# Performance work log

Measured on AMD Instinct MI355X. Metric: run time of the kernel, lower is better.

## Reference

```python
import jax, jax.numpy as jnp
import numpy as np

B, C, H, W = 16, 256, 56, 56
HEADS, DHEAD = 8, 32
INNER = HEADS * DHEAD  # == C
BLOCK, HALO = 7, 3
WIN = BLOCK + 2 * HALO      # 13
REL = WIN                   # rel_size = block + 2*halo
HIDDEN = 4 * C
EPS = 1e-6
LS_INIT = 1e-6


def layernorm2d(x, w, b):
    # channels-first LayerNorm over C, x: (B,C,H,W)
    u = jnp.mean(x, axis=1, keepdims=True)
    s = jnp.mean((x - u) ** 2, axis=1, keepdims=True)
    xn = (x - u) * jax.lax.rsqrt(s + EPS)
    return w[None, :, None, None] * xn + b[None, :, None, None]


def rel_to_abs(x):
    # x: (b, l, 2r-1) -> (b, l, r)
    b, l, m = x.shape
    r = (m + 1) // 2
    x = jnp.pad(x, ((0, 0), (0, 0), (0, 1))).reshape(b, l * (m + 1))
    x = jnp.pad(x, ((0, 0), (0, m - l))).reshape(b, l + 1, m)
    return x[:, :l, -r:]


def relative_logits_1d(q, rel_k):
    # q: (b, h, w, d); rel_k: (2r-1, d) -> (b, h, r, w, r)
    b, h, w, _ = q.shape
    r = (rel_k.shape[0] + 1) // 2
    logits = jnp.einsum('bxyd,rd->bxyr', q, rel_k)
    logits = rel_to_abs(logits.reshape(b * h, w, -1)).reshape(b, h, w, r)
    return jnp.broadcast_to(logits[:, :, None], (b, h, r, w, r))


def rel_pos_bias(q, rel_h, rel_w):
    b = q.shape[0]
    r = (rel_w.shape[0] + 1) // 2
    q2 = q.reshape(b, BLOCK, BLOCK, DHEAD)
    lw = relative_logits_1d(q2, rel_w)                        # (b, x, i, y, j)
    lw = lw.transpose(0, 1, 3, 2, 4).reshape(b, BLOCK * BLOCK, r * r)
    lh = relative_logits_1d(q2.transpose(0, 2, 1, 3), rel_h)  # (b, y, i, x, j)
    lh = lh.transpose(0, 3, 1, 4, 2).reshape(b, BLOCK * BLOCK, r * r)
    return lw + lh


def halo_attention(x, wq, wkv, wo, bo, rel_h, rel_w):
    Bq, _, Hh, Ww = x.shape
    nh, nw = Hh // BLOCK, Ww // BLOCK
    nb = nh * nw
    # queries: non-overlapping blocks -> (B*nb, BLOCK^2, C)
    q_inp = x.reshape(Bq, C, nh, BLOCK, nw, BLOCK).transpose(0, 2, 4, 3, 5, 1)
    q_inp = q_inp.reshape(Bq * nb, BLOCK * BLOCK, C)
    # keys/values: overlapping haloed windows (like F.unfold with padding=HALO)
    xp = jnp.pad(x, ((0, 0), (0, 0), (HALO, HALO), (HALO, HALO)))
    rows = (jnp.arange(nh) * BLOCK)[:, None] + jnp.arange(WIN)
    cols = (jnp.arange(nw) * BLOCK)[:, None] + jnp.arange(WIN)
    kv = xp[:, :, rows][:, :, :, :, cols]
    kv = kv.transpose(0, 2, 4, 3, 5, 1).reshape(Bq * nb, WIN * WIN, C)
    q = q_inp @ wq.T
    k, v = jnp.split(kv @ wkv.T, 2, axis=-1)

    def split_heads(t):
        b2, n2, _ = t.shape
        return t.reshape(b2, n2, HEADS, DHEAD).transpose(0, 2, 1, 3).reshape(b2 * HEADS, n2, DHEAD)

    q, k, v = map(split_heads, (q, k, v))
    q = q * (DHEAD ** -0.5)
    sim = jnp.einsum('bid,bjd->bij', q, k) + rel_pos_bias(q, rel_h, rel_w)
    # mask out-of-bounds (zero-padded) halo positions
    onep = jnp.pad(jnp.ones((Hh, Ww), sim.dtype), ((HALO, HALO), (HALO, HALO)))
    m = (onep[rows][:, :, cols].transpose(0, 2, 1, 3).reshape(nb, WIN * WIN)) > 0
    sim = sim.reshape(Bq, nb, HEADS, BLOCK * BLOCK, WIN * WIN)
    sim = jnp.where(m[None, :, None, None, :], sim, -jnp.finfo(sim.dtype).max)
    sim = sim.reshape(Bq * nb * HEADS, BLOCK * BLOCK, WIN * WIN)
    attn = jax.nn.softmax(sim, axis=-1)
    out = jnp.einsum('bij,bjd->bid', attn, v)
    out = out.reshape(Bq * nb, HEADS, BLOCK * BLOCK, DHEAD).transpose(0, 2, 1, 3)
    out = out.reshape(Bq * nb, BLOCK * BLOCK, INNER) @ wo.T + bo
    out = out.reshape(Bq, nh, nw, BLOCK, BLOCK, C).transpose(0, 5, 1, 3, 2, 4)
    return out.reshape(Bq, C, Hh, Ww)


def _forward(x, ln1_w, ln1_b, ln2_w, ln2_b, wq, wkv, wo, bo, rel_h, rel_w,
             gamma1, gamma2, fc1_w, fc1_b, fc2_w, fc2_b):
    y = halo_attention(layernorm2d(x, ln1_w, ln1_b), wq, wkv, wo, bo, rel_h, rel_w)
    x = x + gamma1 * y  # drop_path = 0 -> identity
    z = layernorm2d(x, ln2_w, ln2_b).transpose(0, 2, 3, 1)  # NHWC
    z = jax.nn.gelu(z @ fc1_w.T + fc1_b, approximate=False)
    z = z @ fc2_w.T + fc2_b
    z = gamma2 * z
    return x + z.transpose(0, 3, 1, 2)


def setup_inputs() -> dict:
    key = jax.random.key(0)
    ks = jax.random.split(key, 8)
    n = lambda k, sh: jax.random.normal(k, sh, jnp.float32) * 0.02
    scale = DHEAD ** -0.5
    return dict(
        x=jax.random.normal(ks[0], (B, C, H, W), jnp.float32),
        ln1_w=jnp.ones((C,), jnp.float32), ln1_b=jnp.zeros((C,), jnp.float32),
        ln2_w=jnp.ones((C,), jnp.float32), ln2_b=jnp.zeros((C,), jnp.float32),
        wq=n(ks[1], (INNER, C)),
        wkv=n(ks[2], (2 * INNER, C)),
        wo=n(ks[3], (C, INNER)), bo=jnp.zeros((C,), jnp.float32),
        rel_h=jax.random.normal(ks[4], (2 * REL - 1, DHEAD), jnp.float32) * scale,
        rel_w=jax.random.normal(ks[5], (2 * REL - 1, DHEAD), jnp.float32) * scale,
        gamma1=jnp.full((1, C, 1, 1), LS_INIT, jnp.float32),
        gamma2=jnp.full((1, 1, 1, C), LS_INIT, jnp.float32),
        fc1_w=n(ks[6], (HIDDEN, C)), fc1_b=jnp.zeros((HIDDEN,), jnp.float32),
        fc2_w=n(ks[7], (C, HIDDEN)), fc2_b=jnp.zeros((C,), jnp.float32),
    )


def reference(x, ln1_w, ln1_b, ln2_w, ln2_b, wq, wkv, wo, bo, rel_h, rel_w,
              gamma1, gamma2, fc1_w, fc1_b, fc2_w, fc2_b):
    return _forward(x, ln1_w, ln1_b, ln2_w, ln2_b, wq, wkv, wo, bo, rel_h, rel_w,
                    gamma1, gamma2, fc1_w, fc1_b, fc2_w, fc2_b)
```

## Files before the change

### kernel.cpp

```cpp
#include <hip/hip_runtime.h>
#include <cmath>

#define DI __device__ __forceinline__

typedef unsigned short ushort_t;
typedef unsigned char u8;
typedef __attribute__((ext_vector_type(8))) short short8;
typedef __attribute__((ext_vector_type(8))) unsigned short ushort8;
typedef __attribute__((ext_vector_type(4))) unsigned short ushort4_t;
typedef __attribute__((ext_vector_type(4))) float floatx4;
typedef unsigned int u32;
typedef __attribute__((ext_vector_type(4))) u32 uintx4;

DI float bf2f(ushort_t u) {
    unsigned v = ((unsigned)u) << 16;
    float f;
    __builtin_memcpy(&f, &v, 4);
    return f;
}
DI ushort_t f2bf(float f) {
    unsigned u;
    __builtin_memcpy(&u, &f, 4);
    unsigned r = (u + 0x7FFFu + ((u >> 16) & 1u)) >> 16;
    return (ushort_t)r;
}
DI ushort_t f2bf_tr(float f) {
    unsigned u;
    __builtin_memcpy(&u, &f, 4);
    return (ushort_t)(u >> 16);
}
DI u32 pack2bf(float lo, float hi) {
    u32 a, b;
    __builtin_memcpy(&a, &lo, 4);
    __builtin_memcpy(&b, &hi, 4);
    return (a >> 16) | (b & 0xFFFF0000u);
}
DI u8 f2e4m3(float f) {
    u32 u;
    __builtin_memcpy(&u, &f, 4);
    u32 s = (u >> 24) & 0x80u;
    u32 a = u & 0x7FFFFFFFu;
    if (a < 0x3C800000u) return (u8)s;
    if (a >= 0x43E00000u) return (u8)(s | 0x7E);
    a += 0x7FFFFu + ((a >> 20) & 1u);
    u32 e = (a >> 23) - 120u;
    u32 m = (a >> 20) & 7u;
    return (u8)(s | (e << 3) | m);
}
DI u8 f2fp8(float v) {
#if __has_builtin(__builtin_amdgcn_cvt_pk_fp8_f32)
    return (u8)(__builtin_amdgcn_cvt_pk_fp8_f32(v, v, 0, false) & 0xFF);
#else
    return f2e4m3(v);
#endif
}
DI u32 pack4fp8(float v0, float v1, float v2, float v3) {
#if __has_builtin(__builtin_amdgcn_cvt_pk_fp8_f32)
    int p = __builtin_amdgcn_cvt_pk_fp8_f32(v0, v1, 0, false);
    p = __builtin_amdgcn_cvt_pk_fp8_f32(v2, v3, p, true);
    return (u32)p;
#else
    return (u32)f2e4m3(v0) | ((u32)f2e4m3(v1) << 8) | ((u32)f2e4m3(v2) << 16) |
           ((u32)f2e4m3(v3) << 24);
#endif
}

DI void async_copy16(const void* gsrc, void* ldst) {
    auto gp = (const __attribute__((address_space(1))) u32*)gsrc;
    auto lp = (__attribute__((address_space(3))) u32*)ldst;
    __builtin_amdgcn_global_load_lds(gp, lp, 16, 0, 0);
}


__global__ void convert_all_kernel(const float* __restrict__ wq, const float* __restrict__ wkv,
                                   const float* __restrict__ wo, const float* __restrict__ fc1w,
                                   const float* __restrict__ fc2w, const float* __restrict__ relh,
                                   const float* __restrict__ relw,
                                   ushort_t* __restrict__ bqkv, ushort_t* __restrict__ woC,
                                   u8* __restrict__ fc1C8, u8* __restrict__ fc2C8,
                                   ushort_t* __restrict__ relC, ushort_t* __restrict__ boneB) {
    int i = blockIdx.x * 256 + threadIdx.x;
    if (i < 196608) { bqkv[i] = f2bf(i < 65536 ? wq[i] : wkv[i - 65536]); return; }
    i -= 196608;
    if (i < 65536) { woC[i] = f2bf(wo[i]); return; }
    i -= 65536;
    if (i < 262144) { fc1C8[i] = f2fp8(fc1w[i]); return; }
    i -= 262144;
    if (i < 262144) { fc2C8[i] = f2fp8(fc2w[i]); return; }
    i -= 262144;
    if (i < 800) { relC[i] = f2bf(relh[i]); return; }
    i -= 800;
    if (i < 800) { relC[800 + i] = f2bf(relw[i]); return; }
    i -= 800;
    if (i < 5632) {
        int j = i >> 5, k = i & 31;
        int kh = j / 13, kw = j - kh * 13;
        ushort_t v = 0;
        if (j < 169) {
            if (k == kh || k == 13 + kw) v = 0x3F80;
            if (k == 28 && kh < 3) v = 0x3F80;
            if (k == 29 && kh >= 10) v = 0x3F80;
            if (k == 30 && kw < 3) v = 0x3F80;
            if (k == 31 && kw >= 10) v = 0x3F80;
        } else {
            if (k == 27) v = 0x3F80;
        }
        boneB[i] = v;
    }
}

__global__ __launch_bounds__(256) void ln1_kernel(const float* __restrict__ x,
                                                  const float* __restrict__ w,
                                                  const float* __restrict__ bias,
                                                  ushort_t* __restrict__ t1) {
    __shared__ __align__(16) float lds[56 * 256];
    int b = blockIdx.x / 56, h = blockIdx.x % 56;
    int c = threadIdx.x;
    const float* row = x + (((size_t)(b * 256 + c) * 56 + h) * 56);
    floatx4 vals[14];
#pragma unroll
    for (int i = 0; i < 14; i++) vals[i] = *(const floatx4*)(row + i * 4);
#pragma unroll
    for (int i = 0; i < 14; i++)
#pragma unroll
        for (int e = 0; e < 4; e++) lds[(i * 4 + e) * 256 + c] = vals[i][e];
    __syncthreads();
    int wv = threadIdx.x >> 6, lane = threadIdx.x & 63;
    for (int p0 = 0; p0 < 14; p0++) {
        int p = wv * 14 + p0;
        float xv[4];
        float s = 0.f, q = 0.f;
#pragma unroll
        for (int j = 0; j < 4; j++) {
            xv[j] = lds[p * 256 + lane * 4 + j];
            s += xv[j];
            q += xv[j] * xv[j];
        }
#pragma unroll
        for (int off = 32; off; off >>= 1) {
            s += __shfl_xor(s, off);
            q += __shfl_xor(q, off);
        }
        float mean = s * (1.f / 256.f);
        float var = q * (1.f / 256.f) - mean * mean;
        float rstd = rsqrtf(var + 1e-6f);
        size_t token = ((size_t)b * 56 + h) * 56 + p;
        ushort4_t o4;
#pragma unroll
        for (int j = 0; j < 4; j++) {
            int cc = lane * 4 + j;
            o4[j] = f2bf_tr(w[cc] * ((xv[j] - mean) * rstd) + bias[cc]);
        }
        *(ushort4_t*)(t1 + token * 256 + lane * 4) = o4;
    }
}

template <int EPI, int F8>
__global__ __launch_bounds__(256) void gemm_kernel(const void* __restrict__ A,
                                                   const void* __restrict__ Bw,
                                                   void* __restrict__ Cout, int K, int N,
                                                   const float* __restrict__ biasf,
                                                   const float* __restrict__ resf,
                                                   const float* __restrict__ gammaf,
                                                   int tok0) {
    constexpr int ES = F8 ? 1 : 2;
    constexpr bool SWAP = (EPI == 6);
    __shared__ __align__(16) char As[2][128 * 32 * ES];
    __shared__ __align__(16) char Bs[2][128 * 32 * ES];
    int gy = gridDim.y;
    int lin = blockIdx.y * gridDim.x + blockIdx.x;
    int chunk = (gridDim.x * gy) >> 3;
    int wl = (lin & 7) * chunk + (lin >> 3);
    int mt = wl / gy;
    int m0 = mt * 128, n0 = (wl - mt * gy) * 128;
    int t = threadIdx.x;
    int wave = t >> 6, lane = t & 63;
    int wm = (wave & 1) * 64, wn = (wave >> 1) * 64;
    int lr = lane & 15, quad = lane >> 4;
    floatx4 acc[4][4] = {};

    const char* A8 = (const char*)A;
    const char* B8 = (const char*)Bw;
    const size_t rbA = (size_t)K * ES;

    int cpr = 2 * ES;
    int r0 = t / cpr, o0 = (t % cpr) * 16;
    int r1 = (t + 256) / cpr, o1 = ((t + 256) % cpr) * 16;
    const char* Ar0 = A8 + (size_t)(m0 + r0) * rbA + o0;
    const char* Br0 = B8 + (size_t)(n0 + r0) * rbA + o0;
    const char* Ar1 = A8 + (size_t)(m0 + r1) * rbA + o1;
    const char* Br1 = B8 + (size_t)(n0 + r1) * rbA + o1;

    async_copy16(Ar0, &As[0][t * 16]);
    async_copy16(Br0, &Bs[0][t * 16]);
    if constexpr (!F8) {
        async_copy16(Ar1, &As[0][(t + 256) * 16]);
        async_copy16(Br1, &Bs[0][(t + 256) * 16]);
    }
    __syncthreads();

    int cur = 0;
    for (int k0 = 0; k0 < K; k0 += 32) {
        if (k0 + 32 < K) {
            size_t nb = (size_t)32 * ES;
            async_copy16(Ar0 + (k0 / 32 + 1) * nb, &As[cur ^ 1][t * 16]);
            async_copy16(Br0 + (k0 / 32 + 1) * nb, &Bs[cur ^ 1][t * 16]);
            if constexpr (!F8) {
                async_copy16(Ar1 + (k0 / 32 + 1) * nb, &As[cur ^ 1][(t + 256) * 16]);
                async_copy16(Br1 + (k0 / 32 + 1) * nb, &Bs[cur ^ 1][(t + 256) * 16]);
            }
        }
        if constexpr (F8) {
            long af[4], bf[4];
#pragma unroll
            for (int i = 0; i < 4; i++)
                __builtin_memcpy(&af[i], &As[cur][(wm + i * 16 + lr) * 32 + quad * 8], 8);
#pragma unroll
            for (int i = 0; i < 4; i++)
                __builtin_memcpy(&bf[i], &Bs[cur][(wn + i * 16 + lr) * 32 + quad * 8], 8);
#pragma unroll
            for (int i = 0; i < 4; i++)
#pragma unroll
                for (int j = 0; j < 4; j++) {
                    if constexpr (SWAP)
                        acc[i][j] = __builtin_amdgcn_mfma_f32_16x16x32_fp8_fp8(bf[j], af[i], acc[i][j], 0, 0, 0);
                    else
                        acc[i][j] = __builtin_amdgcn_mfma_f32_16x16x32_fp8_fp8(af[i], bf[j], acc[i][j], 0, 0, 0);
                }
        } else {
            short8 af[4], bf[4];
#pragma unroll
            for (int i = 0; i < 4; i++) af[i] = *(const short8*)(&As[cur][(wm + i * 16 + lr) * 64 + quad * 16]);
#pragma unroll
            for (int i = 0; i < 4; i++) bf[i] = *(const short8*)(&Bs[cur][(wn + i * 16 + lr) * 64 + quad * 16]);
#pragma unroll
            for (int i = 0; i < 4; i++)
#pragma unroll
                for (int j = 0; j < 4; j++) {
                    if constexpr (SWAP)
                        acc[i][j] = __builtin_amdgcn_mfma_f32_16x16x32_bf16(bf[j], af[i], acc[i][j], 0, 0, 0);
                    else
                        acc[i][j] = __builtin_amdgcn_mfma_f32_16x16x32_bf16(af[i], bf[j], acc[i][j], 0, 0, 0);
                }
        }
        __syncthreads();
        cur ^= 1;
    }
    const float qsc = (EPI == 3 && n0 < 256) ? 0.17677669529663687f : 1.0f;
#pragma unroll
    for (int i = 0; i < 4; i++)
#pragma unroll
        for (int j = 0; j < 4; j++) {
            int row0 = m0 + wm + i * 16 + quad * 4;
            int col = n0 + wn + j * 16 + lr;
            if (EPI == 4) {
                int tokg = tok0 + row0;
                int bb = tokg / 3136;
                int rem = tokg - bb * 3136;
                floatx4 ov;
#pragma unroll
                for (int r = 0; r < 4; r++)
                    ov[r] = resf[(size_t)(row0 + r) * N + col] + gammaf[col] * (acc[i][j][r] + biasf[col]);
                *(floatx4*)((float*)Cout + (size_t)(bb * 256 + col) * 3136 + rem) = ov;
            } else if (EPI == 5) {
                int bb = row0 / 3136;
                int rem = row0 - bb * 3136;
                floatx4 rx = *(const floatx4*)(resf + (size_t)(bb * 256 + col) * 3136 + rem);
#pragma unroll
                for (int r = 0; r < 4; r++)
                    ((float*)Cout)[(size_t)(row0 + r) * N + col] =
                        rx[r] + gammaf[col] * (acc[i][j][r] + biasf[col]);
            } else if (EPI == 6) {
                int mrow = m0 + wm + i * 16 + lr;
                int c0 = n0 + wn + j * 16 + quad * 4;
                floatx4 bi = *(const floatx4*)(biasf + c0);
                float g[4];
#pragma unroll
                for (int r = 0; r < 4; r++) {
                    float v = acc[i][j][r] + bi[r];
                    float hs = fminf(fmaxf(0.3404f * v + 0.5f, 0.0f), 1.0f);
                    g[r] = v * hs;
                }
                *(u32*)((u8*)Cout + (size_t)mrow * N + c0) = pack4fp8(g[0], g[1], g[2], g[3]);
            } else {
#pragma unroll
                for (int r = 0; r < 4; r++)
                    ((ushort_t*)Cout)[(size_t)(row0 + r) * N + col] = f2bf_tr(acc[i][j][r] * qsc);
            }
        }
}

__global__ __launch_bounds__(256, 4) void attn_kernel(const ushort_t* __restrict__ qkv,
                                                      const ushort_t* __restrict__ relh,
                                                      const ushort_t* __restrict__ relw,
                                                      const ushort_t* __restrict__ bone,
                                                      ushort_t* __restrict__ attnout) {
    __shared__ __align__(16) char smem[30208];
    ushort_t* Vt = (ushort_t*)smem;
    ushort_t* tblA = (ushort_t*)(smem + 12800);
    ushort_t* Ks = (ushort_t*)(smem + 16896);
    ushort_t* Ps = (ushort_t*)(smem + 16896);

    int wg = blockIdx.x;
    int head = wg & 7;
    int blk = (wg >> 3) & 63;
    int b = wg >> 9;
    int bh = blk >> 3, bw = blk & 7;
    int t = threadIdx.x;
    int wave = t >> 6, lane = t & 63;
    int lr = lane & 15, quad = lane >> 4;
    const int base_tok = b * 3136;

    short8 bbr[11];
#pragma unroll
    for (int nt = 0; nt < 11; nt++)
        bbr[nt] = *(const short8*)(bone + (nt * 16 + lr) * 32 + quad * 8);
    short8 bfg4[4];
#pragma unroll
    for (int ntile = 0; ntile < 4; ntile++) {
        int n = ntile * 16 + lr;
        int eff = (n < 50) ? n : 0;
        const ushort_t* rp = (eff < 25) ? (relh + eff * 32) : (relw + (eff - 25) * 32);
        bfg4[ntile] = *(const short8*)(rp + quad * 8);
    }
    short8 aq;
    {
        int qrow = wave * 16 + lr;
        int qx = qrow / 7, qy = qrow - qx * 7;
        int tok = min(base_tok + (bh * 7 + qx) * 56 + (bw * 7 + qy), 50175);
        aq = *(const short8*)(qkv + (size_t)tok * 768 + head * 32 + quad * 8);
    }

    ushort8 vv[3];
    int vrow[3], vcol[3];
#pragma unroll
    for (int it = 0; it < 3; it++) {
        int c = t + it * 256;
        bool act = (it < 2) || (t < 192);
        int j = c >> 2, ck = c & 3;
        int kh = j / 13, kw = j - kh * 13;
        int gh = bh * 7 + kh - 3, gw = bw * 7 + kw - 3;
        int tok = min(max(base_tok + gh * 56 + gw, 0), 50175);
        const ushort_t* src = qkv + (size_t)tok * 768 + head * 32 + ck * 8;
        if (act) {
            async_copy16(src + 256, Ks + c * 8);
            vv[it] = *(const ushort8*)(src + 512);
        }
        int nt = j >> 4, l2 = j & 15;
        int col = (nt >= 6) ? (96 + l2 * 6 + nt - 6) : (l2 * 6 + nt);
        vcol[it] = col ^ (ck << 3);
        vrow[it] = ck * 8;
    }
#pragma unroll
    for (int it = 0; it < 3; it++) {
        bool act = (it < 2) || (t < 192);
        if (act) {
#pragma unroll
            for (int e = 0; e < 8; e++) Vt[(vrow[it] + e) * 200 + vcol[it]] = vv[it][e];
        }
    }
#pragma unroll
    for (int i = 0; i < 2; i++) {
        int idx = t + i * 256;
        int row = idx >> 4, l2 = idx & 15;
        int col = 96 + l2 * 6 + 5;
        Vt[row * 200 + (col ^ ((row >> 3) << 3))] = 0;
    }
    {
        const u32 NEG = 0xCE6Eu;
        bool himask = (t & 3) == 3;
        u32 e1 = himask ? (NEG << 16) : 0u;
        u32 e2m = himask ? ((bh == 0 ? NEG : 0u) | (bh == 7 ? NEG << 16 : 0u)) : 0u;
        u32 e3m = himask ? ((bw == 0 ? NEG : 0u) | (bw == 7 ? NEG << 16 : 0u)) : 0u;
        uintx4 ini = {0u, e1, e2m, e3m};
        *(uintx4*)(smem + 12800 + t * 16) = ini;
    }
    __syncthreads();

    floatx4 zero4 = {0.f, 0.f, 0.f, 0.f};

    int qx_r[4], qy_r[4];
#pragma unroll
    for (int r = 0; r < 4; r++) {
        int row = wave * 16 + quad * 4 + r;
        qx_r[r] = row / 7;
        qy_r[r] = row - qx_r[r] * 7;
    }

#pragma unroll
    for (int ntile = 0; ntile < 4; ntile++) {
        int n = ntile * 16 + lr;
        floatx4 cta = __builtin_amdgcn_mfma_f32_16x16x32_bf16(aq, bfg4[ntile], zero4, 0, 0, 0);
#pragma unroll
        for (int r = 0; r < 4; r++) {
            int slot = (n < 25) ? (n - 12 + qx_r[r]) : (n - 24 + qy_r[r]);
            bool ok = (n < 25) ? (slot >= 0 && slot <= 12)
                               : (n < 50 && slot >= 13 && slot <= 25);
            int ss = ok ? slot : 26;
            tblA[(wave * 16 + quad * 4 + r) * 32 + ss] = f2bf_tr(cta[r]);
        }
    }

    short8 afb = *(const short8*)(tblA + (wave * 16 + lr) * 32 + quad * 8);
    floatx4 sacc[11];
#pragma unroll
    for (int nt = 0; nt < 11; nt++) {
        short8 bk = *(const short8*)(Ks + (nt * 16 + lr) * 32 + quad * 8);
        floatx4 s0 = __builtin_amdgcn_mfma_f32_16x16x32_bf16(aq, bk, zero4, 0, 0, 0);
        sacc[nt] = __builtin_amdgcn_mfma_f32_16x16x32_bf16(afb, bbr[nt], s0, 0, 0, 0);
    }

    __syncthreads();

    u32 phi[4][3];
#pragma unroll
    for (int r = 0; r < 4; r++) {
        int qr2 = wave * 16 + quad * 4 + r;
        float eb[11];
#pragma unroll
        for (int nt = 0; nt < 11; nt++) eb[nt] = __expf(sacc[nt][r]);
        u32* prow = (u32*)(Ps + qr2 * 104 + lr * 6);
        prow[0] = pack2bf(eb[0], eb[1]);
        prow[1] = pack2bf(eb[2], eb[3]);
        prow[2] = pack2bf(eb[4], eb[5]);
        phi[r][0] = pack2bf(eb[6], eb[7]);
        phi[r][1] = pack2bf(eb[8], eb[9]);
        phi[r][2] = pack2bf(eb[10], 0.f);
    }

    short8 ones8;
#pragma unroll
    for (int e = 0; e < 8; e++) ones8[e] = (short)0x3F80;

    floatx4 oacc[2] = {zero4, zero4};
    floatx4 osum = zero4;
#pragma unroll
    for (int kk = 0; kk < 3; kk++) {
        int k0 = kk * 32;
        short8 ap = *(const short8*)(Ps + (wave * 16 + lr) * 104 + k0 + quad * 8);
#pragma unroll
        for (int n2 = 0; n2 < 2; n2++) {
            int d = n2 * 16 + lr;
            int colb = (k0 + quad * 8) ^ ((d >> 3) << 3);
            short8 bv = *(const short8*)(Vt + d * 200 + colb);
            oacc[n2] = __builtin_amdgcn_mfma_f32_16x16x32_bf16(ap, bv, oacc[n2], 0, 0, 0);
        }
        osum = __builtin_amdgcn_mfma_f32_16x16x32_bf16(ap, ones8, osum, 0, 0, 0);
    }
#pragma unroll
    for (int r = 0; r < 4; r++) {
        int qr2 = wave * 16 + quad * 4 + r;
        u32* prow = (u32*)(Ps + qr2 * 104 + lr * 6);
        prow[0] = phi[r][0];
        prow[1] = phi[r][1];
        prow[2] = phi[r][2];
    }
#pragma unroll
    for (int kk = 0; kk < 3; kk++) {
        int k0 = kk * 32;
        short8 ap = *(const short8*)(Ps + (wave * 16 + lr) * 104 + k0 + quad * 8);
#pragma unroll
        for (int n2 = 0; n2 < 2; n2++) {
            int d = n2 * 16 + lr;
            int colb = (96 + k0 + quad * 8) ^ ((d >> 3) << 3);
            short8 bv = *(const short8*)(Vt + d * 200 + colb);
            oacc[n2] = __builtin_amdgcn_mfma_f32_16x16x32_bf16(ap, bv, oacc[n2], 0, 0, 0);
        }
        osum = __builtin_amdgcn_mfma_f32_16x16x32_bf16(ap, ones8, osum, 0, 0, 0);
    }

#pragma unroll
    for (int n2 = 0; n2 < 2; n2++)
#pragma unroll
        for (int r = 0; r < 4; r++) {
            int qr2 = wave * 16 + quad * 4 + r;
            if (qr2 < 49) {
                float inv = __builtin_amdgcn_rcpf(osum[r]);
                int qx = qr2 / 7, qy = qr2 - qx * 7;
                size_t tok = (size_t)base_tok + (bh * 7 + qx) * 56 + (bw * 7 + qy);
                attnout[tok * 256 + head * 32 + n2 * 16 + lr] = f2bf_tr(oacc[n2][r] * inv);
            }
        }
}

__global__ __launch_bounds__(256) void ln2_kernel(const float* __restrict__ xin,
                                                  const float* __restrict__ w,
                                                  const float* __restrict__ bias,
                                                  u8* __restrict__ o) {
    int token = blockIdx.x * 4 + (threadIdx.x >> 6);
    int lane = threadIdx.x & 63;
    floatx4 v4 = *(const floatx4*)(xin + (size_t)token * 256 + lane * 4);
    float s = 0.f, q = 0.f;
#pragma unroll
    for (int i = 0; i < 4; i++) {
        s += v4[i];
        q += v4[i] * v4[i];
    }
#pragma unroll
    for (int off = 32; off; off >>= 1) {
        s += __shfl_xor(s, off);
        q += __shfl_xor(q, off);
    }
    float mean = s * (1.f / 256.f);
    float var = q * (1.f / 256.f) - mean * mean;
    float rstd = rsqrtf(var + 1e-6f);
    float g[4];
#pragma unroll
    for (int i = 0; i < 4; i++) {
        int c = lane * 4 + i;
        g[i] = w[c] * ((v4[i] - mean) * rstd) + bias[c];
    }
    *(u32*)(o + (size_t)token * 256 + lane * 4) = pack4fp8(g[0], g[1], g[2], g[3]);
}

extern "C" void kernel_launch(void* const* d_in, const int* in_sizes, int n_in,
                              void* d_out, int out_size, void* d_ws, size_t ws_size,
                              hipStream_t stream) {
    const float* x = (const float*)d_in[0];
    const float* ln1w = (const float*)d_in[1];
    const float* ln1b = (const float*)d_in[2];
    const float* ln2w = (const float*)d_in[3];
    const float* ln2b = (const float*)d_in[4];
    const float* wq = (const float*)d_in[5];
    const float* wkv = (const float*)d_in[6];
    const float* wo = (const float*)d_in[7];
    const float* bo = (const float*)d_in[8];
    const float* relh = (const float*)d_in[9];
    const float* relw = (const float*)d_in[10];
    const float* g1 = (const float*)d_in[11];
    const float* g2 = (const float*)d_in[12];
    const float* fc1w = (const float*)d_in[13];
    const float* fc1b = (const float*)d_in[14];
    const float* fc2w = (const float*)d_in[15];
    const float* fc2b = (const float*)d_in[16];
    float* out = (float*)d_out;

    char* ws = (char*)d_ws;
    float* x1 = (float*)ws;
    ushort_t* t1 = (ushort_t*)(ws + 51380224);
    ushort_t* attnb = t1;
    ushort_t* qkv = (ushort_t*)(ws + 77070336);
    u8* t2 = (u8*)qkv;
    u8* hid8 = (u8*)(ws + 102760448);
    ushort_t* wv_ = (ushort_t*)(ws + 154140672);
    ushort_t* bqkv = wv_;
    ushort_t* woC = wv_ + 196608;
    u8* fc1C8 = (u8*)(woC + 65536);
    u8* fc2C8 = (u8*)(woC + 65536 + 262144);
    ushort_t* relC = woC + 65536 + 262144 + 131072;
    ushort_t* boneG = relC + 1600;

    convert_all_kernel<<<3101, 256, 0, stream>>>(wq, wkv, wo, fc1w, fc2w, relh, relw,
                                                 bqkv, woC, fc1C8, fc2C8, relC, boneG);
    ln1_kernel<<<896, 256, 0, stream>>>(x, ln1w, ln1b, t1);
    gemm_kernel<3, 0><<<dim3(392, 6), 256, 0, stream>>>(t1, bqkv, qkv, 256, 768, nullptr, nullptr, nullptr, 0);
    attn_kernel<<<8192, 256, 0, stream>>>(qkv, relC, relC + 800, boneG, attnb);
    gemm_kernel<5, 0><<<dim3(392, 2), 256, 0, stream>>>(attnb, woC, x1, 256, 256, bo, x, g1, 0);
    ln2_kernel<<<12544, 256, 0, stream>>>(x1, ln2w, ln2b, t2);
    gemm_kernel<6, 1><<<dim3(392, 8), 256, 0, stream>>>(t2, fc1C8, hid8, 256, 1024, fc1b, nullptr, nullptr, 0);
    gemm_kernel<4, 1><<<dim3(392, 2), 256, 0, stream>>>(hid8, fc2C8, out, 1024, 256, fc2b, x1, g2, 0);
}
```

Measured before the change: 386.1 us.

## Move QKV and output projections to FP8 and load full K into LDS

The LN1 output, attention output, QKV weights and output-projection weights are now quantized to FP8 instead of bf16, so the QKV and Wo GEMMs use FP8 MFMA and move half the bytes. The K=256 GEMMs are replaced by a kernel that loads the whole 256-wide K slab into LDS in one pass, removing the per-step double-buffer syncs. FC2 gets its own specialized pipelined kernel. This trades accuracy, since activations feeding attention now use e4m3, and the larger LDS footprint may lower occupancy.

```diff
diff --git a/kernel.cpp b/kernel.cpp
--- a/kernel.cpp
+++ b/kernel.cpp
@@ -76,13 +76,13 @@
                                    const float* __restrict__ wo, const float* __restrict__ fc1w,
                                    const float* __restrict__ fc2w, const float* __restrict__ relh,
                                    const float* __restrict__ relw,
-                                   ushort_t* __restrict__ bqkv, ushort_t* __restrict__ woC,
+                                   u8* __restrict__ bqkv8, u8* __restrict__ woC8,
                                    u8* __restrict__ fc1C8, u8* __restrict__ fc2C8,
                                    ushort_t* __restrict__ relC, ushort_t* __restrict__ boneB) {
     int i = blockIdx.x * 256 + threadIdx.x;
-    if (i < 196608) { bqkv[i] = f2bf(i < 65536 ? wq[i] : wkv[i - 65536]); return; }
+    if (i < 196608) { bqkv8[i] = f2fp8(i < 65536 ? wq[i] : wkv[i - 65536]); return; }
     i -= 196608;
-    if (i < 65536) { woC[i] = f2bf(wo[i]); return; }
+    if (i < 65536) { woC8[i] = f2fp8(wo[i]); return; }
     i -= 65536;
     if (i < 262144) { fc1C8[i] = f2fp8(fc1w[i]); return; }
     i -= 262144;
@@ -112,7 +112,7 @@
 __global__ __launch_bounds__(256) void ln1_kernel(const float* __restrict__ x,
                                                   const float* __restrict__ w,
                                                   const float* __restrict__ bias,
-                                                  ushort_t* __restrict__ t1) {
+                                                  u8* __restrict__ t1) {
     __shared__ __align__(16) float lds[56 * 256];
     int b = blockIdx.x / 56, h = blockIdx.x % 56;
     int c = threadIdx.x;
@@ -145,28 +145,26 @@
         float var = q * (1.f / 256.f) - mean * mean;
         float rstd = rsqrtf(var + 1e-6f);
         size_t token = ((size_t)b * 56 + h) * 56 + p;
-        ushort4_t o4;
+        float g[4];
 #pragma unroll
         for (int j = 0; j < 4; j++) {
             int cc = lane * 4 + j;
-            o4[j] = f2bf_tr(w[cc] * ((xv[j] - mean) * rstd) + bias[cc]);
-        }
-        *(ushort4_t*)(t1 + token * 256 + lane * 4) = o4;
-    }
-}
-
-template <int EPI, int F8>
-__global__ __launch_bounds__(256) void gemm_kernel(const void* __restrict__ A,
-                                                   const void* __restrict__ Bw,
-                                                   void* __restrict__ Cout, int K, int N,
-                                                   const float* __restrict__ biasf,
-                                                   const float* __restrict__ resf,
-                                                   const float* __restrict__ gammaf,
-                                                   int tok0) {
-    constexpr int ES = F8 ? 1 : 2;
+            g[j] = w[cc] * ((xv[j] - mean) * rstd) + bias[cc];
+        }
+        *(u32*)(t1 + token * 256 + lane * 4) = pack4fp8(g[0], g[1], g[2], g[3]);
+    }
+}
+
+template <int EPI>
+__global__ __launch_bounds__(256) void gemm_fullk_kernel(const u8* __restrict__ A,
+                                                         const u8* __restrict__ Bw,
+                                                         void* __restrict__ Cout, int N,
+                                                         const float* __restrict__ biasf,
+                                                         const float* __restrict__ resf,
+                                                         const float* __restrict__ gammaf) {
     constexpr bool SWAP = (EPI == 6);
-    __shared__ __align__(16) char As[2][128 * 32 * ES];
-    __shared__ __align__(16) char Bs[2][128 * 32 * ES];
+    __shared__ __align__(16) u8 As[32768];
+    __shared__ __align__(16) u8 Bs[32768];
     int gy = gridDim.y;
     int lin = blockIdx.y * gridDim.x + blockIdx.x;
     int chunk = (gridDim.x * gy) >> 3;
@@ -179,73 +177,36 @@
     int lr = lane & 15, quad = lane >> 4;
     floatx4 acc[4][4] = {};
 
-    const char* A8 = (const char*)A;
-    const char* B8 = (const char*)Bw;
-    const size_t rbA = (size_t)K * ES;
-
-    int cpr = 2 * ES;
-    int r0 = t / cpr, o0 = (t % cpr) * 16;
-    int r1 = (t + 256) / cpr, o1 = ((t + 256) % cpr) * 16;
-    const char* Ar0 = A8 + (size_t)(m0 + r0) * rbA + o0;
-    const char* Br0 = B8 + (size_t)(n0 + r0) * rbA + o0;
-    const char* Ar1 = A8 + (size_t)(m0 + r1) * rbA + o1;
-    const char* Br1 = B8 + (size_t)(n0 + r1) * rbA + o1;
-
-    async_copy16(Ar0, &As[0][t * 16]);
-    async_copy16(Br0, &Bs[0][t * 16]);
-    if constexpr (!F8) {
-        async_copy16(Ar1, &As[0][(t + 256) * 16]);
-        async_copy16(Br1, &Bs[0][(t + 256) * 16]);
+#pragma unroll
+    for (int it = 0; it < 8; it++) {
+        int g = it * 256 + t;
+        int kt = g >> 8, w = g & 255;
+        int row = w >> 1, c16 = (w & 1) * 16;
+        async_copy16(A + (size_t)(m0 + row) * 256 + kt * 32 + c16, As + g * 16);
+        async_copy16(Bw + (size_t)(n0 + row) * 256 + kt * 32 + c16, Bs + g * 16);
     }
     __syncthreads();
 
-    int cur = 0;
-    for (int k0 = 0; k0 < K; k0 += 32) {
-        if (k0 + 32 < K) {
-            size_t nb = (size_t)32 * ES;
-            async_copy16(Ar0 + (k0 / 32 + 1) * nb, &As[cur ^ 1][t * 16]);
-            async_copy16(Br0 + (k0 / 32 + 1) * nb, &Bs[cur ^ 1][t * 16]);
-            if constexpr (!F8) {
-                async_copy16(Ar1 + (k0 / 32 + 1) * nb, &As[cur ^ 1][(t + 256) * 16]);
-                async_copy16(Br1 + (k0 / 32 + 1) * nb, &Bs[cur ^ 1][(t + 256) * 16]);
+#pragma unroll
+    for (int kt = 0; kt < 8; kt++) {
+        long af[4], bf[4];
+#pragma unroll
+        for (int i = 0; i < 4; i++)
+            __builtin_memcpy(&af[i], &As[kt * 4096 + (wm + i * 16 + lr) * 32 + quad * 8], 8);
+#pragma unroll
+        for (int i = 0; i < 4; i++)
+            __builtin_memcpy(&bf[i], &Bs[kt * 4096 + (wn + i * 16 + lr) * 32 + quad * 8], 8);
+#pragma unroll
+        for (int i = 0; i < 4; i++)
+#pragma unroll
+            for (int j = 0; j < 4; j++) {
+                if constexpr (SWAP)
+                    acc[i][j] = __builtin_amdgcn_mfma_f32_16x16x32_fp8_fp8(bf[j], af[i], acc[i][j], 0, 0, 0);
+                else
+                    acc[i][j] = __builtin_amdgcn_mfma_f32_16x16x32_fp8_fp8(af[i], bf[j], acc[i][j], 0, 0, 0);
             }
-        }
-        if constexpr (F8) {
-            long af[4], bf[4];
-#pragma unroll
-            for (int i = 0; i < 4; i++)
-                __builtin_memcpy(&af[i], &As[cur][(wm + i * 16 + lr) * 32 + quad * 8], 8);
-#pragma unroll
-            for (int i = 0; i < 4; i++)
-                __builtin_memcpy(&bf[i], &Bs[cur][(wn + i * 16 + lr) * 32 + quad * 8], 8);
-#pragma unroll
-            for (int i = 0; i < 4; i++)
-#pragma unroll
-                for (int j = 0; j < 4; j++) {
-                    if constexpr (SWAP)
-                        acc[i][j] = __builtin_amdgcn_mfma_f32_16x16x32_fp8_fp8(bf[j], af[i], acc[i][j], 0, 0, 0);
-                    else
-                        acc[i][j] = __builtin_amdgcn_mfma_f32_16x16x32_fp8_fp8(af[i], bf[j], acc[i][j], 0, 0, 0);
-                }
-        } else {
-            short8 af[4], bf[4];
-#pragma unroll
-            for (int i = 0; i < 4; i++) af[i] = *(const short8*)(&As[cur][(wm + i * 16 + lr) * 64 + quad * 16]);
-#pragma unroll
-            for (int i = 0; i < 4; i++) bf[i] = *(const short8*)(&Bs[cur][(wn + i * 16 + lr) * 64 + quad * 16]);
-#pragma unroll
-            for (int i = 0; i < 4; i++)
-#pragma unroll
-                for (int j = 0; j < 4; j++) {
-                    if constexpr (SWAP)
-                        acc[i][j] = __builtin_amdgcn_mfma_f32_16x16x32_bf16(bf[j], af[i], acc[i][j], 0, 0, 0);
-                    else
-                        acc[i][j] = __builtin_amdgcn_mfma_f32_16x16x32_bf16(af[i], bf[j], acc[i][j], 0, 0, 0);
-                }
-        }
-        __syncthreads();
-        cur ^= 1;
-    }
+    }
+
     const float qsc = (EPI == 3 && n0 < 256) ? 0.17677669529663687f : 1.0f;
 #pragma unroll
     for (int i = 0; i < 4; i++)
@@ -253,16 +214,7 @@
         for (int j = 0; j < 4; j++) {
             int row0 = m0 + wm + i * 16 + quad * 4;
             int col = n0 + wn + j * 16 + lr;
-            if (EPI == 4) {
-                int tokg = tok0 + row0;
-                int bb = tokg / 3136;
-                int rem = tokg - bb * 3136;
-                floatx4 ov;
-#pragma unroll
-                for (int r = 0; r < 4; r++)
-                    ov[r] = resf[(size_t)(row0 + r) * N + col] + gammaf[col] * (acc[i][j][r] + biasf[col]);
-                *(floatx4*)((float*)Cout + (size_t)(bb * 256 + col) * 3136 + rem) = ov;
-            } else if (EPI == 5) {
+            if (EPI == 5) {
                 int bb = row0 / 3136;
                 int rem = row0 - bb * 3136;
                 floatx4 rx = *(const floatx4*)(resf + (size_t)(bb * 256 + col) * 3136 + rem);
@@ -290,11 +242,76 @@
         }
 }
 
+__global__ __launch_bounds__(256) void gemm_fc2_kernel(const u8* __restrict__ A,
+                                                       const u8* __restrict__ Bw,
+                                                       float* __restrict__ Cout, int K, int N,
+                                                       const float* __restrict__ biasf,
+                                                       const float* __restrict__ resf,
+                                                       const float* __restrict__ gammaf) {
+    __shared__ __align__(16) u8 As[2][128 * 32];
+    __shared__ __align__(16) u8 Bs[2][128 * 32];
+    int gy = gridDim.y;
+    int lin = blockIdx.y * gridDim.x + blockIdx.x;
+    int chunk = (gridDim.x * gy) >> 3;
+    int wl = (lin & 7) * chunk + (lin >> 3);
+    int mt = wl / gy;
+    int m0 = mt * 128, n0 = (wl - mt * gy) * 128;
+    int t = threadIdx.x;
+    int wave = t >> 6, lane = t & 63;
+    int wm = (wave & 1) * 64, wn = (wave >> 1) * 64;
+    int lr = lane & 15, quad = lane >> 4;
+    floatx4 acc[4][4] = {};
+
+    int r0 = t >> 1, o0 = (t & 1) * 16;
+    const u8* Ar0 = A + (size_t)(m0 + r0) * K + o0;
+    const u8* Br0 = Bw + (size_t)(n0 + r0) * K + o0;
+
+    async_copy16(Ar0, &As[0][t * 16]);
+    async_copy16(Br0, &Bs[0][t * 16]);
+    __syncthreads();
+
+    int cur = 0;
+    for (int k0 = 0; k0 < K; k0 += 32) {
+        if (k0 + 32 < K) {
+            async_copy16(Ar0 + k0 + 32, &As[cur ^ 1][t * 16]);
+            async_copy16(Br0 + k0 + 32, &Bs[cur ^ 1][t * 16]);
+        }
+        long af[4], bf[4];
+#pragma unroll
+        for (int i = 0; i < 4; i++)
+            __builtin_memcpy(&af[i], &As[cur][(wm + i * 16 + lr) * 32 + quad * 8], 8);
+#pragma unroll
+        for (int i = 0; i < 4; i++)
+            __builtin_memcpy(&bf[i], &Bs[cur][(wn + i * 16 + lr) * 32 + quad * 8], 8);
+#pragma unroll
+        for (int i = 0; i < 4; i++)
+#pragma unroll
+            for (int j = 0; j < 4; j++)
+                acc[i][j] = __builtin_amdgcn_mfma_f32_16x16x32_fp8_fp8(af[i], bf[j], acc[i][j], 0, 0, 0);
+        __syncthreads();
+        cur ^= 1;
+    }
+#pragma unroll
+    for (int i = 0; i < 4; i++)
+#pragma unroll
+        for (int j = 0; j < 4; j++) {
+            int row0 = m0 + wm + i * 16 + quad * 4;
+            int col = n0 + wn + j * 16 + lr;
+            int bb = row0 / 3136;
+            int rem = row0 - bb * 3136;
+            floatx4 ov;
+#pragma unroll
+            for (int r = 0; r < 4; r++)
+                ov[r] = resf[(size_t)(row0 + r) * N + col] + gammaf[col] * (acc[i][j][r] + biasf[col]);
+            *(floatx4*)(Cout + (size_t)(bb * 256 + col) * 3136 + rem) = ov;
+        }
+}
+
 __global__ __launch_bounds__(256, 4) void attn_kernel(const ushort_t* __restrict__ qkv,
                                                       const ushort_t* __restrict__ relh,
                                                       const ushort_t* __restrict__ relw,
                                                       const ushort_t* __restrict__ bone,
-                                                      ushort_t* __restrict__ attnout) {
+                                                      u8* __restrict__ attnout) {
     __shared__ __align__(16) char smem[30208];
     ushort_t* Vt = (ushort_t*)smem;
     ushort_t* tblA = (ushort_t*)(smem + 12800);
@@ -478,7 +495,7 @@
                 float inv = __builtin_amdgcn_rcpf(osum[r]);
                 int qx = qr2 / 7, qy = qr2 - qx * 7;
                 size_t tok = (size_t)base_tok + (bh * 7 + qx) * 56 + (bw * 7 + qy);
-                attnout[tok * 256 + head * 32 + n2 * 16 + lr] = f2bf_tr(oacc[n2][r] * inv);
+                attnout[tok * 256 + head * 32 + n2 * 16 + lr] = f2fp8(oacc[n2][r] * inv);
             }
         }
 }
@@ -537,26 +554,26 @@
 
     char* ws = (char*)d_ws;
     float* x1 = (float*)ws;
-    ushort_t* t1 = (ushort_t*)(ws + 51380224);
-    ushort_t* attnb = t1;
+    u8* t18 = (u8*)(ws + 51380224);
+    u8* attnb = t18;
     ushort_t* qkv = (ushort_t*)(ws + 77070336);
     u8* t2 = (u8*)qkv;
     u8* hid8 = (u8*)(ws + 102760448);
-    ushort_t* wv_ = (ushort_t*)(ws + 154140672);
-    ushort_t* bqkv = wv_;
-    ushort_t* woC = wv_ + 196608;
-    u8* fc1C8 = (u8*)(woC + 65536);
-    u8* fc2C8 = (u8*)(woC + 65536 + 262144);
-    ushort_t* relC = woC + 65536 + 262144 + 131072;
+    char* wv_ = ws + 154140672;
+    u8* bqkv8 = (u8*)wv_;
+    u8* woC8 = (u8*)(wv_ + 196608);
+    u8* fc1C8 = (u8*)(wv_ + 262144);
+    u8* fc2C8 = (u8*)(wv_ + 524288);
+    ushort_t* relC = (ushort_t*)(wv_ + 786432);
     ushort_t* boneG = relC + 1600;
 
     convert_all_kernel<<<3101, 256, 0, stream>>>(wq, wkv, wo, fc1w, fc2w, relh, relw,
-                                                 bqkv, woC, fc1C8, fc2C8, relC, boneG);
-    ln1_kernel<<<896, 256, 0, stream>>>(x, ln1w, ln1b, t1);
-    gemm_kernel<3, 0><<<dim3(392, 6), 256, 0, stream>>>(t1, bqkv, qkv, 256, 768, nullptr, nullptr, nullptr, 0);
+                                                 bqkv8, woC8, fc1C8, fc2C8, relC, boneG);
+    ln1_kernel<<<896, 256, 0, stream>>>(x, ln1w, ln1b, t18);
+    gemm_fullk_kernel<3><<<dim3(392, 6), 256, 0, stream>>>(t18, bqkv8, qkv, 768, nullptr, nullptr, nullptr);
     attn_kernel<<<8192, 256, 0, stream>>>(qkv, relC, relC + 800, boneG, attnb);
-    gemm_kernel<5, 0><<<dim3(392, 2), 256, 0, stream>>>(attnb, woC, x1, 256, 256, bo, x, g1, 0);
+    gemm_fullk_kernel<5><<<dim3(392, 2), 256, 0, stream>>>(attnb, woC8, x1, 256, bo, x, g1);
     ln2_kernel<<<12544, 256, 0, stream>>>(x1, ln2w, ln2b, t2);
-    gemm_kernel<6, 1><<<dim3(392, 8), 256, 0, stream>>>(t2, fc1C8, hid8, 256, 1024, fc1b, nullptr, nullptr, 0);
-    gemm_kernel<4, 1><<<dim3(392, 2), 256, 0, stream>>>(hid8, fc2C8, out, 1024, 256, fc2b, x1, g2, 0);
-}
+    gemm_fullk_kernel<6><<<dim3(392, 8), 256, 0, stream>>>(t2, fc1C8, hid8, 1024, fc1b, nullptr, nullptr);
+    gemm_fc2_kernel<<<dim3(392, 2), 256, 0, stream>>>(hid8, fc2C8, out, 1024, 256, fc2b, x1, g2);
+}
```

Result: faster. 361.3 us (-6.4%).
